# Kernel optimization log

Measured on AMD Instinct MI355X. Metric: run time of the kernel, lower is better.

## Reference

```python
import jax, jax.numpy as jnp
import numpy as np

H, DH = 8, 64
DIM = 512
INNER = H * DH
GAMMA = 0.01
LAMBDA_REG = 0.001


def _ln(x, g, b, eps=1e-5):
    mu = x.mean(-1, keepdims=True)
    var = x.var(-1, keepdims=True)  # ddof=0, matches torch LayerNorm
    return (x - mu) / jnp.sqrt(var + eps) * g + b


def _proj(x, ln_g, ln_b, W):
    # LayerNorm -> Linear(no bias) -> split heads: [Q,N,DIM] -> [H,Q,N,DH]
    Q, N, _ = x.shape
    y = _ln(x, ln_g, ln_b) @ W
    return jnp.transpose(y.reshape(Q, N, H, DH), (2, 0, 1, 3))


def setup_inputs() -> dict:
    key = jax.random.key(0)
    ks = jax.random.split(key, 10)
    s = 0.02
    return {
        "q": jax.random.normal(ks[0], (16, 512, DIM), jnp.float32),
        "k": jax.random.normal(ks[1], (16, 512, DIM), jnp.float32),
        "v": jax.random.normal(ks[2], (16, 512, DIM), jnp.float32),
        "ln_g": jnp.ones((DIM,), jnp.float32),
        "ln_b": jnp.zeros((DIM,), jnp.float32),
        "W_in": jax.random.normal(ks[3], (DIM, INNER), jnp.float32) * s,
        "wp1_w": jax.random.normal(ks[4], (2 * DH, DH), jnp.float32) * s,
        "wp1_b": jnp.zeros((DH,), jnp.float32),
        "wpln_g": jnp.ones((DH,), jnp.float32),
        "wpln_b": jnp.zeros((DH,), jnp.float32),
        "wp2_w": jax.random.normal(ks[5], (DH, DH // 2), jnp.float32) * s,
        "wp2_b": jnp.zeros((DH // 2,), jnp.float32),
        "wp3_w": jax.random.normal(ks[6], (DH // 2, 3), jnp.float32) * s,
        "wp3_b": jnp.zeros((3,), jnp.float32),
        "temp": jnp.ones((1,), jnp.float32) * 5.0,
        "W_out": jax.random.normal(ks[7], (INNER, DIM), jnp.float32) * s,
        "b_out": jnp.zeros((DIM,), jnp.float32),
    }


def reference(q, k, v, ln_g, ln_b, W_in, wp1_w, wp1_b, wpln_g, wpln_b,
              wp2_w, wp2_b, wp3_w, wp3_b, temp, W_out, b_out):
    sg = jax.lax.stop_gradient
    std1 = lambda x: jnp.std(x, ddof=1)  # torch.std is unbiased

    f_q = _proj(q, ln_g, ln_b, W_in)  # [H,Q,N,DH]
    f_k = _proj(k, ln_g, ln_b, W_in)  # [H,Q,M,DH]
    f_v = _proj(v, ln_g, ln_b, W_in)
    m = f_k.shape[2]

    # --- cosine similarity component (cosine_distance + extra clamp) ---
    dots_raw = jnp.einsum('hqnd,hqmd->hqnm', f_q, f_k)
    n1 = jnp.linalg.norm(f_q, axis=-1, keepdims=True) + 1e-8          # [H,Q,N,1]
    n2 = jnp.linalg.norm(f_k, axis=-1, keepdims=True) + 1e-8          # [H,Q,M,1]
    cosine_sim = jnp.clip(dots_raw / (n1 * jnp.swapaxes(n2, -1, -2)), -0.99, 0.99)

    # --- regularized covariance component ---
    f_kc = f_k - f_k.mean(axis=2, keepdims=True)
    f_qc = f_q - f_q.mean(axis=-1, keepdims=True)
    cov = jnp.einsum('hqnd,hqmd->hqnm', f_qc, f_kc) / (DH ** 0.5 + 1e-8)
    cov = jnp.clip((LAMBDA_REG / max(m, 1)) * cov, -10.0, 10.0)

    # --- margin-based variance component (eval mode: adaptive_gamma == GAMMA) ---
    fqn = f_q / jnp.maximum(jnp.linalg.norm(f_q, axis=-1, keepdims=True), 1e-8)
    fkn = f_k / jnp.maximum(jnp.linalg.norm(f_k, axis=-1, keepdims=True), 1e-8)
    cs = jnp.clip(jnp.einsum('hqnd,hqmd->hqnm', fqn, fkn), -0.99, 0.99)
    margin = jnp.clip(GAMMA - cs, 0.0, 2.0)
    var_comp = jnp.broadcast_to(margin.mean(-1, keepdims=True), cs.shape)

    # --- dynamic weight predictor (dropouts identity in eval) ---
    qg = f_q.mean(axis=(1, 2))                 # [H,DH]
    kg = f_k.mean(axis=(1, 2))
    feats = jnp.concatenate([qg, kg], axis=-1)  # [H,2*DH]
    h1 = jax.nn.relu(_ln(feats @ wp1_w + wp1_b, wpln_g, wpln_b))
    h2 = jax.nn.relu(h1 @ wp2_w + wp2_b)
    logits = jax.nn.softmax(h2 @ wp3_w + wp3_b, axis=-1)  # softmax inside Sequential
    weights = jax.nn.softmax(logits / jnp.clip(temp, 0.1, 20.0), axis=-1)  # [H,3]
    cos_w = weights[:, 0].reshape(H, 1, 1, 1)
    cov_w = weights[:, 1].reshape(H, 1, 1, 1)
    var_w = weights[:, 2].reshape(H, 1, 1, 1)

    # --- global-std rescale + mix + adaptive temperature ---
    cos_s = cosine_sim / (sg(std1(cosine_sim)) + 1e-8)
    cov_s = cov / (sg(std1(cov)) + 1e-8) * 0.1
    var_s = var_comp / (sg(std1(var_comp)) + 1e-8) * 0.1
    dots = cos_w * cos_s + cov_w * cov_s + var_w * var_s
    attn_t = 1.0 + 0.5 * sg(std1(dots))
    dots = dots / jnp.clip(attn_t, 0.5, 5.0)

    out = jnp.einsum('hqnm,hqmd->hqnd', jax.nn.softmax(dots, axis=-1), f_v)
    out = jnp.transpose(out, (1, 2, 0, 3)).reshape(q.shape[0], q.shape[1], INNER)
    return out @ W_out + b_out
```

## Files before the change

### kernel.cpp

```cpp
#include <hip/hip_runtime.h>
#include <math.h>

#define NH 8
#define DHD 64
#define DMODEL 512
#define QB 16
#define SEQ 512
#define NROWS (QB*SEQ)
#define NHQ (NH*QB)
#define KCOV ((float)((0.001/512.0)/(8.0+1e-8)))

typedef __attribute__((ext_vector_type(8))) short short8;
typedef __attribute__((ext_vector_type(8))) unsigned short ushort8v;
typedef __attribute__((ext_vector_type(4))) unsigned short ushort4v;
typedef __attribute__((ext_vector_type(4))) float f32x4;

__device__ __forceinline__ float bf2f(unsigned short u){
  union { unsigned int i; float f; } c; c.i = ((unsigned int)u)<<16; return c.f;
}
__device__ __forceinline__ unsigned short f2bf(float f){
  union { float f; unsigned int i; } c; c.f = f;
  unsigned int u = c.i;
  u += 0x7fffu + ((u>>16)&1u);
  return (unsigned short)(u>>16);
}
__device__ __forceinline__ unsigned cvtpk(float a, float b){
  unsigned r; asm("v_cvt_pk_bf16_f32 %0, %1, %2" : "=v"(r) : "v"(a), "v"(b)); return r;
}
__device__ __forceinline__ float clampf(float x, float lo, float hi){ return fminf(fmaxf(x,lo),hi); }

__device__ __forceinline__ f32x4 MFMA(short8 a, short8 b, f32x4 c){
  return __builtin_amdgcn_mfma_f32_16x16x32_bf16(a, b, c, 0, 0, 0);
}
__device__ __forceinline__ short8 frag_ld(const unsigned short* T, int row, int rowbytes, int kbyte){
  int addr = row*rowbytes + (kbyte ^ ((row&7)<<4));
  return *reinterpret_cast<const short8*>(reinterpret_cast<const char*>(T) + addr);
}
__device__ __forceinline__ void tile_st16(unsigned short* T, int row, int rowbytes, int kbyte, ushort8v v){
  int addr = row*rowbytes + (kbyte ^ ((row&7)<<4));
  *reinterpret_cast<ushort8v*>(reinterpret_cast<char*>(T) + addr) = v;
}
__device__ __forceinline__ void tile_st8(unsigned short* T, int row, int rowbytes, int kbyte, ushort4v v){
  int addr = row*rowbytes + (kbyte ^ ((row&7)<<4));
  *reinterpret_cast<ushort4v*>(reinterpret_cast<char*>(T) + addr) = v;
}

__global__ void __launch_bounds__(256) prep_kernel(
    const float* __restrict__ xq, const float* __restrict__ xk, const float* __restrict__ xv,
    const float* __restrict__ Wi, const float* __restrict__ Wo,
    float* __restrict__ mu, float* __restrict__ rstd,
    unsigned short* __restrict__ WiT, unsigned short* __restrict__ WoT)
{
  __shared__ float T[64][68];
  int b = blockIdx.x, t = threadIdx.x;
  if (b < 6144){
    int which = b >> 11, rowblk = b & 2047;
    const float* src = which==0 ? xq : (which==1 ? xk : xv);
    int w = t >> 6, lane = t & 63;
    int row = rowblk*4 + w;
    const float* x = src + (size_t)row*DMODEL;
    float4 v1 = *reinterpret_cast<const float4*>(&x[lane*8]);
    float4 v2 = *reinterpret_cast<const float4*>(&x[lane*8+4]);
    float s  = v1.x+v1.y+v1.z+v1.w + v2.x+v2.y+v2.z+v2.w;
    float ss = v1.x*v1.x+v1.y*v1.y+v1.z*v1.z+v1.w*v1.w
             + v2.x*v2.x+v2.y*v2.y+v2.z*v2.z+v2.w*v2.w;
    #pragma unroll
    for (int m=32; m>0; m>>=1){ s += __shfl_xor(s,m,64); ss += __shfl_xor(ss,m,64); }
    if (lane==0){
      float m_ = s*(1.0f/DMODEL);
      float var = ss*(1.0f/DMODEL) - m_*m_;
      mu[(size_t)which*NROWS + row]   = m_;
      rstd[(size_t)which*NROWS + row] = rsqrtf(var + 1e-5f);
    }
  } else {
    int wb = b - 6144;
    const float* src = (wb>=64) ? Wo : Wi;
    unsigned short* dst = (wb>=64) ? WoT : WiT;
    int rc = wb & 63;
    int r0 = (rc>>3)*64, c0 = (rc&7)*64;
    for (int it=0; it<4; ++it){
      int idx = it*256+t, row = idx>>4, q = idx&15;
      float4 v = *reinterpret_cast<const float4*>(&src[(size_t)(r0+row)*DMODEL + c0 + q*4]);
      T[row][q*4+0]=v.x; T[row][q*4+1]=v.y; T[row][q*4+2]=v.z; T[row][q*4+3]=v.w;
    }
    __syncthreads();
    for (int it=0; it<4; ++it){
      int idx = it*256+t, oc = idx>>4, q = idx&15;
      ushort4v o;
      o[0]=f2bf(T[q*4+0][oc]); o[1]=f2bf(T[q*4+1][oc]);
      o[2]=f2bf(T[q*4+2][oc]); o[3]=f2bf(T[q*4+3][oc]);
      *reinterpret_cast<ushort4v*>(&dst[(size_t)(c0+oc)*DMODEL + r0 + q*4]) = o;
    }
  }
}

__global__ void __launch_bounds__(256) proj_mfma_kernel(
    const float* __restrict__ xq, const float* __restrict__ xk, const float* __restrict__ xv,
    const float* __restrict__ g, const float* __restrict__ bb,
    const unsigned short* __restrict__ WiT,
    const float* __restrict__ mu, const float* __restrict__ rstd,
    unsigned short* __restrict__ fq, unsigned short* __restrict__ fk, unsigned short* __restrict__ fvT,
    float* __restrict__ aqA, float* __restrict__ i1qA,
    float* __restrict__ rskA, float* __restrict__ i1kA)
{
  int which = blockIdx.z;
  const float* src = which==0?xq:(which==1?xk:xv);
  int r0 = blockIdx.x*128;
  int c0 = blockIdx.y*128;
  __shared__ unsigned short XT[128*64];
  __shared__ unsigned short WT[128*64];
  __shared__ float gs[DMODEL], bs[DMODEL], mus[128], rss[128];
  int t = threadIdx.x;
  for (int i=t;i<DMODEL;i+=256){ gs[i]=g[i]; bs[i]=bb[i]; }
  if (t<128){ mus[t]=mu[(size_t)which*NROWS+r0+t]; rss[t]=rstd[(size_t)which*NROWS+r0+t]; }
  int w=t>>6, lane=t&63, l16=lane&15, lh=lane>>4;
  f32x4 acc[4][4];
  #pragma unroll
  for(int i=0;i<4;i++){ for(int j=0;j<4;j++) acc[i][j]=(f32x4){0.f,0.f,0.f,0.f}; }
  for (int k0=0;k0<DMODEL;k0+=64){
    __syncthreads();
    for (int it=0; it<8; ++it){
      int idx=it*256+t, row=idx>>4, q=idx&15;
      float4 x4 = *reinterpret_cast<const float4*>(&src[(size_t)(r0+row)*DMODEL + k0 + q*4]);
      float m_=mus[row], rs_=rss[row];
      const float* g4=&gs[k0+q*4]; const float* b4=&bs[k0+q*4];
      ushort4v o;
      o[0]=f2bf((x4.x-m_)*rs_*g4[0]+b4[0]);
      o[1]=f2bf((x4.y-m_)*rs_*g4[1]+b4[1]);
      o[2]=f2bf((x4.z-m_)*rs_*g4[2]+b4[2]);
      o[3]=f2bf((x4.w-m_)*rs_*g4[3]+b4[3]);
      tile_st8(XT, row, 128, q*8, o);
    }
    for (int it=0; it<4; ++it){
      int idx=it*256+t, row=idx>>3, q=idx&7;
      ushort8v v = *reinterpret_cast<const ushort8v*>(&WiT[(size_t)(c0+row)*DMODEL + k0 + q*8]);
      tile_st16(WT, row, 128, q*16, v);
    }
    __syncthreads();
    if (which<2){
      int dr=(w&1)*64, nc=(w>>1)*64;
      #pragma unroll
      for (int ks=0; ks<2; ++ks){
        int kb = lh*16 + ks*64;
        short8 a[4], b[4];
        #pragma unroll
        for (int i=0;i<4;i++) a[i] = frag_ld(WT, dr+i*16+l16, 128, kb);
        #pragma unroll
        for (int j=0;j<4;j++) b[j] = frag_ld(XT, nc+j*16+l16, 128, kb);
        #pragma unroll
        for (int i=0;i<4;i++){
          #pragma unroll
          for (int j=0;j<4;j++) acc[i][j]=MFMA(a[i],b[j],acc[i][j]);
        }
      }
    } else {
      int nr=(w>>1)*64, dc=(w&1)*64;
      #pragma unroll
      for (int ks=0; ks<2; ++ks){
        int kb = lh*16 + ks*64;
        short8 a[4], b[4];
        #pragma unroll
        for (int i=0;i<4;i++) a[i] = frag_ld(XT, nr+i*16+l16, 128, kb);
        #pragma unroll
        for (int j=0;j<4;j++) b[j] = frag_ld(WT, dc+j*16+l16, 128, kb);
        #pragma unroll
        for (int i=0;i<4;i++){
          #pragma unroll
          for (int j=0;j<4;j++) acc[i][j]=MFMA(a[i],b[j],acc[i][j]);
        }
      }
    }
  }
  if (which<2){
    unsigned short* dst = which ? fk : fq;
    int dr=(w&1)*64, nc=(w>>1)*64;
    #pragma unroll
    for (int i=0;i<4;i++){
      #pragma unroll
      for (int j=0;j<4;j++){
        int cl = c0 + dr + i*16 + lh*4;
        int ng = r0 + nc + j*16 + l16;
        int head = cl>>6, dd = cl&63;
        int hq = head*QB + (ng>>9);
        int n = ng&511;
        ushort4v o;
        o[0]=f2bf(acc[i][j][0]); o[1]=f2bf(acc[i][j][1]);
        o[2]=f2bf(acc[i][j][2]); o[3]=f2bf(acc[i][j][3]);
        *reinterpret_cast<ushort4v*>(&dst[((size_t)hq*SEQ+n)*DHD + dd]) = o;
      }
    }
    int head = (c0>>6) + (w&1);
    #pragma unroll
    for (int j=0;j<4;j++){
      float s=0.f, ss=0.f;
      #pragma unroll
      for (int i=0;i<4;i++){
        #pragma unroll
        for (int r=0;r<4;r++){ float x = acc[i][j][r]; s += x; ss = fmaf(x,x,ss); }
      }
      s += __shfl_xor(s,16,64); ss += __shfl_xor(ss,16,64);
      s += __shfl_xor(s,32,64); ss += __shfl_xor(ss,32,64);
      if (lh==0){
        int ng = r0 + nc + j*16 + l16;
        int hq = head*QB + (ng>>9);
        int n = ng&511;
        float nrm = sqrtf(ss);
        if (which==0){
          aqA[hq*SEQ+n]  = s*(1.0f/64.0f);
          i1qA[hq*SEQ+n] = 1.0f/(nrm+1e-8f);
        } else {
          rskA[hq*SEQ+n] = s;
          i1kA[hq*SEQ+n] = 1.0f/(nrm+1e-8f);
        }
      }
    }
  } else {
    int nr=(w>>1)*64, dc=(w&1)*64;
    #pragma unroll
    for (int i=0;i<4;i++){
      #pragma unroll
      for (int j=0;j<4;j++){
        int ngb = r0 + nr + i*16 + lh*4;
        int dg  = c0 + dc + j*16 + l16;
        int head = dg>>6, dd = dg&63;
        int hq = head*QB + (ngb>>9);
        int n = ngb&511;
        ushort4v o;
        o[0]=f2bf(acc[i][j][0]); o[1]=f2bf(acc[i][j][1]);
        o[2]=f2bf(acc[i][j][2]); o[3]=f2bf(acc[i][j][3]);
        *reinterpret_cast<ushort4v*>(&fvT[((size_t)hq*DHD+dd)*SEQ + n]) = o;
      }
    }
  }
}

__global__ void __launch_bounds__(256) colsum_kernel(
    const unsigned short* __restrict__ fq, const unsigned short* __restrict__ fk,
    float* __restrict__ colpart)
{
  int hq = blockIdx.x, quarter = blockIdx.y, isk = blockIdx.z;
  const unsigned short* F = (isk ? fk : fq) + (size_t)hq*SEQ*DHD;
  int t = threadIdx.x, g = t&15, rg = t>>4;
  float acc0=0.f, acc1=0.f, acc2=0.f, acc3=0.f;
  #pragma unroll
  for (int i=0;i<8;i++){
    int r = quarter*128 + rg + 16*i;
    ushort4v v = *reinterpret_cast<const ushort4v*>(&F[(size_t)r*DHD + g*4]);
    acc0+=bf2f(v[0]); acc1+=bf2f(v[1]); acc2+=bf2f(v[2]); acc3+=bf2f(v[3]);
  }
  __shared__ float sh[16][68];
  sh[rg][g*4+0]=acc0; sh[rg][g*4+1]=acc1; sh[rg][g*4+2]=acc2; sh[rg][g*4+3]=acc3;
  __syncthreads();
  if (t<64){
    float s=0.f;
    #pragma unroll
    for (int r=0;r<16;r++) s += sh[r][t];
    colpart[(((size_t)isk*NHQ + hq)*4 + quarter)*64 + t] = s;
  }
}

__global__ void __launch_bounds__(64) colreduce_kernel(
    const float* __restrict__ colpart,
    float* __restrict__ qgp, float* __restrict__ kgp, float* __restrict__ c2A)
{
  int hq = blockIdx.x, d = threadIdx.x;
  float sq=0.f, sk=0.f;
  #pragma unroll
  for (int qu=0;qu<4;qu++){
    sq += colpart[(((size_t)0*NHQ + hq)*4 + qu)*64 + d];
    sk += colpart[(((size_t)1*NHQ + hq)*4 + qu)*64 + d];
  }
  qgp[hq*64+d]=sq; kgp[hq*64+d]=sk;
  float c = sk*(1.0f/512.0f);
  #pragma unroll
  for (int m=32;m>0;m>>=1) c += __shfl_xor(c,m,64);
  if (d==0) c2A[hq]=c;
}

__global__ void __launch_bounds__(256) score_m1_kernel(
    const unsigned short* __restrict__ fq, const unsigned short* __restrict__ fk,
    const float* __restrict__ aqA, const float* __restrict__ i1qA,
    const float* __restrict__ rskA, const float* __restrict__ i1kA,
    const float* __restrict__ c2A, const float* __restrict__ kgp,
    float* __restrict__ c1A, float* __restrict__ rmaxcA, float* __restrict__ rmaxoA,
    float* __restrict__ momf, double* __restrict__ varp)
{
  int strip=blockIdx.x, q_=blockIdx.y, h=blockIdx.z;
  int hq=h*QB+q_, n0=strip*64;
  const unsigned short* Fq=fq+(size_t)hq*SEQ*DHD;
  const unsigned short* Fk=fk+(size_t)hq*SEQ*DHD;
  __shared__ unsigned short KT[128*64];
  __shared__ float red[256];
  __shared__ double dred[256];
  int t=threadIdx.x, w=t>>6, lane=t&63, l16=lane&15, lh=lane>>4;
  int n = n0 + w*16 + l16;
  float c2v = c2A[hq];
  float aqv = aqA[hq*SEQ+n];
  float iq1 = i1qA[hq*SEQ+n];
  short8 qa[2];
  #pragma unroll
  for (int ks=0;ks<2;ks++)
    qa[ks] = *reinterpret_cast<const short8*>(&Fq[(size_t)n*DHD + ks*32 + lh*8]);
  float c1v = 0.f;
  #pragma unroll
  for (int ks=0;ks<2;ks++){
    const float* bkp = &kgp[hq*64 + ks*32 + lh*8];
    float4 b0 = *reinterpret_cast<const float4*>(bkp);
    float4 b1 = *reinterpret_cast<const float4*>(bkp+4);
    float bb[8] = {b0.x,b0.y,b0.z,b0.w,b1.x,b1.y,b1.z,b1.w};
    #pragma unroll
    for (int i=0;i<8;i++) c1v = fmaf(bf2f((unsigned short)qa[ks][i]), bb[i], c1v);
  }
  c1v *= (1.0f/512.0f);
  c1v += __shfl_xor(c1v,16,64);
  c1v += __shfl_xor(c1v,32,64);
  if (lane<16) c1A[hq*SEQ+n] = c1v;
  float c1x = KCOV*(c1v - aqv*c2v);
  float aqx = KCOV*aqv;
  float sc=0.f,sc2=0.f,so=0.f,so2=0.f,sco=0.f;
  float rc=0.f, ro=0.f, rm=0.f, rmc=-1e30f, rmo=-1e30f;
  for (int mc=0;mc<4;mc++){
    int m0=mc*128;
    __syncthreads();
    for (int it=0;it<4;++it){
      int idx=it*256+t, row=idx>>3, qc=idx&7;
      ushort8v vv = *reinterpret_cast<const ushort8v*>(&Fk[(size_t)(m0+row)*DHD + qc*8]);
      tile_st16(KT,row,128,qc*16,vv);
    }
    __syncthreads();
    #pragma unroll
    for (int mh=0;mh<2;mh++){
      int mb = mh*64;
      f32x4 acc[4];
      #pragma unroll
      for (int mf=0;mf<4;mf++) acc[mf]=(f32x4){0.f,0.f,0.f,0.f};
      #pragma unroll
      for (int mf=0;mf<4;mf++){
        #pragma unroll
        for (int ks=0;ks<2;ks++){
          short8 kf = frag_ld(KT, mb+mf*16+l16, 128, lh*16+ks*64);
          acc[mf] = MFMA(kf, qa[ks], acc[mf]);
        }
      }
      #pragma unroll
      for (int mf=0;mf<4;mf++){
        int mg = hq*SEQ + m0 + mb + mf*16 + lh*4;
        float4 rsk4 = *reinterpret_cast<const float4*>(&rskA[mg]);
        float4 i1k4 = *reinterpret_cast<const float4*>(&i1kA[mg]);
        float rk[4]={rsk4.x,rsk4.y,rsk4.z,rsk4.w};
        float ik[4]={i1k4.x,i1k4.y,i1k4.z,i1k4.w};
        #pragma unroll
        for (int r=0;r<4;r++){
          float S = acc[mf][r];
          float cosv = clampf(S*iq1*ik[r], -0.99f, 0.99f);
          float u = fmaf(KCOV, S, -c1x);
          float covv = fmaf(-aqx, rk[r], u);
          covv = clampf(covv, -10.0f, 10.0f);
          float marg = clampf(0.01f - cosv, 0.0f, 2.0f);
          sc += cosv; sc2 = fmaf(cosv,cosv,sc2);
          so += covv; so2 = fmaf(covv,covv,so2);
          sco = fmaf(cosv,covv,sco);
          rc += cosv; ro += covv; rm += marg;
          rmc = fmaxf(rmc, cosv); rmo = fmaxf(rmo, covv);
        }
      }
    }
  }
  rc += __shfl_xor(rc,16,64); rc += __shfl_xor(rc,32,64);
  ro += __shfl_xor(ro,16,64); ro += __shfl_xor(ro,32,64);
  rm += __shfl_xor(rm,16,64); rm += __shfl_xor(rm,32,64);
  rmc = fmaxf(rmc, __shfl_xor(rmc,16,64)); rmc = fmaxf(rmc, __shfl_xor(rmc,32,64));
  rmo = fmaxf(rmo, __shfl_xor(rmo,16,64)); rmo = fmaxf(rmo, __shfl_xor(rmo,32,64));
  if (lane<16){
    rmaxcA[hq*SEQ+n] = rmc;
    rmaxoA[hq*SEQ+n] = rmo;
  }
  double vm=0.0, vm2=0.0, vmc=0.0, vmo=0.0;
  if (lane<16){
    float mm = rm*(1.0f/512.0f);
    vm  = (double)mm;
    vm2 = (double)mm*(double)mm;
    vmc = (double)mm*(double)rc;
    vmo = (double)mm*(double)ro;
  }
  float fs[5]={sc,sc2,so,so2,sco};
  for (int c=0;c<5;c++){
    __syncthreads();
    red[t]=fs[c]; __syncthreads();
    for (int o=128;o>0;o>>=1){ if (t<o) red[t]+=red[t+o]; __syncthreads(); }
    if (t==0) momf[(size_t)(hq*8+strip)*5 + c] = red[0];
  }
  double ds[4]={vm,vm2,vmc,vmo};
  for (int c=0;c<4;c++){
    __syncthreads();
    dred[t]=ds[c]; __syncthreads();
    for (int o=128;o>0;o>>=1){ if (t<o) dred[t]+=dred[t+o]; __syncthreads(); }
    if (t==0) varp[(size_t)(hq*8+strip)*4 + c] = dred[0];
  }
}

__global__ void __launch_bounds__(256) finalize_kernel(
    const float* __restrict__ qgp, const float* __restrict__ kgp,
    const float* __restrict__ wp1w, const float* __restrict__ wp1b,
    const float* __restrict__ wplg, const float* __restrict__ wplb,
    const float* __restrict__ wp2w, const float* __restrict__ wp2b,
    const float* __restrict__ wp3w, const float* __restrict__ wp3b,
    const float* __restrict__ temp,
    const float* __restrict__ momf, const double* __restrict__ varp,
    float* __restrict__ params)
{
  int t = threadIdx.x;
  __shared__ float feats[8][128];
  __shared__ float h1s[8][64];
  __shared__ float h2s[8][32];
  __shared__ float wts[8][3];
  __shared__ double Sh[8][9];
  for (int idx=t; idx<512; idx+=256){
    int h = idx>>6, d = idx&63;
    float s1=0, s2=0;
    for (int qq=0; qq<QB; qq++){ s1 += qgp[(h*QB+qq)*64+d]; s2 += kgp[(h*QB+qq)*64+d]; }
    feats[h][d]    = s1*(1.0f/8192.0f);
    feats[h][64+d] = s2*(1.0f/8192.0f);
  }
  __syncthreads();
  int w = t>>6, j = t&63;
  for (int pp=0; pp<2; pp++){
    int h = w + pp*4;
    float acc = wp1b[j];
    for (int k=0;k<128;k++) acc += feats[h][k]*wp1w[k*64+j];
    float s=acc, s2=acc*acc;
    #pragma unroll
    for (int m=32;m>0;m>>=1){ s+=__shfl_xor(s,m,64); s2+=__shfl_xor(s2,m,64); }
    float mean = s*(1.0f/64.0f);
    float var  = s2*(1.0f/64.0f) - mean*mean;
    float xh = (acc-mean)*rsqrtf(var+1e-5f)*wplg[j] + wplb[j];
    h1s[h][j] = fmaxf(xh, 0.0f);
  }
  __syncthreads();
  {
    int h = t>>5, j2 = t&31;
    float acc = wp2b[j2];
    for (int k=0;k<64;k++) acc += h1s[h][k]*wp2w[k*32+j2];
    h2s[h][j2] = fmaxf(acc, 0.0f);
  }
  __syncthreads();
  if (t<8){
    int h = t;
    float z[3] = {wp3b[0], wp3b[1], wp3b[2]};
    for (int k=0;k<32;k++){
      float hv = h2s[h][k];
      z[0]+=hv*wp3w[k*3]; z[1]+=hv*wp3w[k*3+1]; z[2]+=hv*wp3w[k*3+2];
    }
    float mx = fmaxf(z[0], fmaxf(z[1], z[2]));
    float e0=expf(z[0]-mx), e1=expf(z[1]-mx), e2=expf(z[2]-mx);
    float inv = 1.0f/(e0+e1+e2);
    float l0=e0*inv, l1=e1*inv, l2=e2*inv;
    float tv = temp[0]; tv = fminf(fmaxf(tv, 0.1f), 20.0f);
    float y0=l0/tv, y1=l1/tv, y2=l2/tv;
    float mx2 = fmaxf(y0, fmaxf(y1, y2));
    float f0=expf(y0-mx2), f1=expf(y1-mx2), f2=expf(y2-mx2);
    float inv2 = 1.0f/(f0+f1+f2);
    wts[h][0]=f0*inv2; wts[h][1]=f1*inv2; wts[h][2]=f2*inv2;
  }
  __syncthreads();
  if (t<40){
    int h = t/5, c = t%5;
    double s = 0;
    for (int e=0; e<128; e++) s += (double)momf[(size_t)(h*128+e)*5 + c];
    Sh[h][c] = s;
  }
  __syncthreads();
  if (t<32){
    int h = t>>2, c = t&3;
    double s = 0;
    for (int e=0; e<128; e++) s += varp[(size_t)(h*128+e)*4 + c];
    Sh[h][5+c] = s;
  }
  __syncthreads();
  if (t==0){
    const double Ntot = 33554432.0;
    double T1c=0,T2c=0,T1o=0,T2o=0,T1v=0,T2v=0;
    for (int h=0;h<8;h++){
      T1c+=Sh[h][0]; T2c+=Sh[h][1]; T1o+=Sh[h][2]; T2o+=Sh[h][3];
      T1v+=512.0*Sh[h][5]; T2v+=512.0*Sh[h][6];
    }
    double stdc = sqrt(fmax((T2c - T1c*T1c/Ntot)/(Ntot-1.0), 0.0));
    double stdo = sqrt(fmax((T2o - T1o*T1o/Ntot)/(Ntot-1.0), 0.0));
    double stdv = sqrt(fmax((T2v - T1v*T1v/Ntot)/(Ntot-1.0), 0.0));
    double ah[8], bh[8];
    double Sd1=0, Sd2=0;
    for (int h=0;h<8;h++){
      double a = (double)wts[h][0]/(stdc+1e-8);
      double b = (double)wts[h][1]*0.1/(stdo+1e-8);
      double c = (double)wts[h][2]*0.1/(stdv+1e-8);
      ah[h]=a; bh[h]=b;
      Sd1 += a*Sh[h][0] + b*Sh[h][2] + c*512.0*Sh[h][5];
      Sd2 += a*a*Sh[h][1] + b*b*Sh[h][3] + c*c*512.0*Sh[h][6]
           + 2.0*a*b*Sh[h][4] + 2.0*a*c*Sh[h][7] + 2.0*b*c*Sh[h][8];
    }
    double stdd = sqrt(fmax((Sd2 - Sd1*Sd1/Ntot)/(Ntot-1.0), 0.0));
    double att = 1.0 + 0.5*stdd;
    att = fmin(fmax(att, 0.5), 5.0);
    double scale = 1.0/att;
    for (int h=0;h<8;h++){
      params[h*2+0] = (float)(scale*ah[h]);
      params[h*2+1] = (float)(scale*bh[h]);
    }
  }
}

__global__ void __launch_bounds__(256) attn_m2_kernel(
    const unsigned short* __restrict__ fq, const unsigned short* __restrict__ fk,
    const unsigned short* __restrict__ fvT,
    const float* __restrict__ aqA, const float* __restrict__ c1A, const float* __restrict__ i1qA,
    const float* __restrict__ rskA, const float* __restrict__ i1kA,
    const float* __restrict__ c2A, const float* __restrict__ params,
    const float* __restrict__ rmaxcA, const float* __restrict__ rmaxoA,
    unsigned short* __restrict__ attn_bf)
{
  int strip=blockIdx.x, q_=blockIdx.y, h=blockIdx.z;
  int hq=h*QB+q_, n0=strip*64;
  const unsigned short* Fq=fq+(size_t)hq*SEQ*DHD;
  const unsigned short* Fk=fk+(size_t)hq*SEQ*DHD;
  const unsigned short* FvT=fvT+(size_t)hq*DHD*SEQ;
  __shared__ unsigned short KT[128*64];
  __shared__ unsigned short VT[64*128];
  __shared__ unsigned short P[64*64];
  int t=threadIdx.x, w=t>>6, lane=t&63, l16=lane&15, lh=lane>>4;
  int n = n0 + w*16 + l16;
  float c2v=c2A[hq];
  float pa=params[h*2], pb=params[h*2+1];
  float aqv = aqA[hq*SEQ+n];
  float c1v = c1A[hq*SEQ+n];
  float iq1 = i1qA[hq*SEQ+n];
  float rmc = rmaxcA[hq*SEQ+n];
  float rmo = rmaxoA[hq*SEQ+n];
  float pbk = pb*KCOV;
  float ra  = pa*iq1;
  float bndc = 0.99f*pa;
  float rowc = -pbk*(c1v - aqv*c2v);
  float r3   = pbk*aqv;
  float Mrow = fmaf(pa, rmc, pb*rmo);
  short8 qa[2];
  #pragma unroll
  for (int ks=0;ks<2;ks++)
    qa[ks] = *reinterpret_cast<const short8*>(&Fq[(size_t)n*DHD + ks*32 + lh*8]);
  short8 ones;
  #pragma unroll
  for (int i=0;i<8;i++) ones[i] = (short)0x3F80;
  f32x4 accO[4];
  #pragma unroll
  for (int j=0;j<4;j++) accO[j]=(f32x4){0.f,0.f,0.f,0.f};
  f32x4 den = (f32x4){0.f,0.f,0.f,0.f};
  for (int mc=0;mc<4;mc++){
    int m0=mc*128;
    __syncthreads();
    for (int it=0;it<4;++it){
      int idx=it*256+t, row=idx>>3, qc=idx&7;
      ushort8v vv = *reinterpret_cast<const ushort8v*>(&Fk[(size_t)(m0+row)*DHD + qc*8]);
      tile_st16(KT,row,128,qc*16,vv);
    }
    for (int it=0;it<4;++it){
      int idx=it*256+t, dd=idx>>4, c=idx&15;
      ushort8v vv=*reinterpret_cast<const ushort8v*>(&FvT[(size_t)dd*SEQ + m0 + c*8]);
      tile_st16(VT, dd, 256, c*16, vv);
    }
    __syncthreads();
    #pragma unroll
    for (int mh=0;mh<2;mh++){
      int mb = mh*64;
      f32x4 acc[4];
      #pragma unroll
      for (int mf=0;mf<4;mf++) acc[mf]=(f32x4){0.f,0.f,0.f,0.f};
      #pragma unroll
      for (int mf=0;mf<4;mf++){
        #pragma unroll
        for (int ks=0;ks<2;ks++){
          short8 kf = frag_ld(KT, mb+mf*16+l16, 128, lh*16+ks*64);
          acc[mf] = MFMA(kf, qa[ks], acc[mf]);
        }
      }
      int prow = w*16 + l16;
      #pragma unroll
      for (int mf=0;mf<4;mf++){
        int mg = hq*SEQ + m0 + mb + mf*16 + lh*4;
        float4 rsk4 = *reinterpret_cast<const float4*>(&rskA[mg]);
        float4 i1k4 = *reinterpret_cast<const float4*>(&i1kA[mg]);
        float rk[4]={rsk4.x,rsk4.y,rsk4.z,rsk4.w};
        float ik[4]={i1k4.x,i1k4.y,i1k4.z,i1k4.w};
        #pragma unroll
        for (int r=0;r<4;r++){
          float S = acc[mf][r];
          float tt = S*ra; tt *= ik[r];
          float cc = clampf(tt, -bndc, bndc);
          float u = fmaf(pbk, S, rowc);
          float lin = fmaf(-r3, rk[r], u);
          acc[mf][r] = __expf(cc + lin - Mrow);
        }
        unsigned lo = cvtpk(acc[mf][0], acc[mf][1]);
        unsigned hi = cvtpk(acc[mf][2], acc[mf][3]);
        int pbyte = (mf*32 + lh*8) ^ ((prow&7)<<4);
        *reinterpret_cast<uint2*>(reinterpret_cast<char*>(P) + prow*128 + pbyte)
          = make_uint2(lo, hi);
      }
      #pragma unroll
      for (int ks=0;ks<2;ks++){
        short8 pfrag = frag_ld(P, prow, 128, lh*16 + ks*64);
        #pragma unroll
        for (int dcf=0;dcf<4;dcf++){
          short8 vb = frag_ld(VT, dcf*16+l16, 256, mb*2 + ks*64 + lh*16);
          accO[dcf] = MFMA(pfrag, vb, accO[dcf]);
        }
        den = MFMA(pfrag, ones, den);
      }
    }
  }
  f32x4 invD;
  #pragma unroll
  for (int r=0;r<4;r++) invD[r] = 1.0f/den[r];
  #pragma unroll
  for (int dcf=0;dcf<4;dcf++){
    #pragma unroll
    for (int r=0;r<4;r++){
      int row = w*16 + lh*4 + r;
      int col = dcf*16 + l16;
      int addr = row*128 + ((col*2) ^ ((row&7)<<4));
      *reinterpret_cast<unsigned short*>(reinterpret_cast<char*>(P) + addr)
        = f2bf(accO[dcf][r]*invD[r]);
    }
  }
  __syncthreads();
  for (int it=0; it<2; ++it){
    int idx = it*256 + t;
    int row = idx>>3, c = idx&7;
    int addr = row*128 + ((c*16) ^ ((row&7)<<4));
    ushort8v vv = *reinterpret_cast<ushort8v*>(reinterpret_cast<char*>(P) + addr);
    *reinterpret_cast<ushort8v*>(
      &attn_bf[(size_t)(q_*SEQ + n0 + row)*DMODEL + h*DHD + c*8]) = vv;
  }
}

__global__ void __launch_bounds__(256) out_mfma_kernel(
    const unsigned short* __restrict__ attn_bf, const unsigned short* __restrict__ WoT,
    const float* __restrict__ bias, float* __restrict__ out)
{
  int r0=blockIdx.x*128;
  int c0=blockIdx.y*128;
  __shared__ unsigned short AT[128*64];
  __shared__ unsigned short WT[128*64];
  int t=threadIdx.x, w=t>>6, lane=t&63, l16=lane&15, lh=lane>>4;
  f32x4 acc[4][4];
  #pragma unroll
  for(int i=0;i<4;i++){ for(int j=0;j<4;j++) acc[i][j]=(f32x4){0.f,0.f,0.f,0.f}; }
  for (int k0=0;k0<DMODEL;k0+=64){
    __syncthreads();
    for (int it=0; it<4; ++it){
      int idx=it*256+t, row=idx>>3, q=idx&7;
      ushort8v v = *reinterpret_cast<const ushort8v*>(&attn_bf[(size_t)(r0+row)*DMODEL + k0 + q*8]);
      tile_st16(AT, row, 128, q*16, v);
    }
    for (int it=0; it<4; ++it){
      int idx=it*256+t, row=idx>>3, q=idx&7;
      ushort8v v = *reinterpret_cast<const ushort8v*>(&WoT[(size_t)(c0+row)*DMODEL + k0 + q*8]);
      tile_st16(WT, row, 128, q*16, v);
    }
    __syncthreads();
    int nr=(w&1)*64, mr=(w>>1)*64;
    #pragma unroll
    for (int ks=0; ks<2; ++ks){
      int kb = lh*16 + ks*64;
      short8 a[4], b[4];
      #pragma unroll
      for (int i=0;i<4;i++) a[i] = frag_ld(WT, nr+i*16+l16, 128, kb);
      #pragma unroll
      for (int j=0;j<4;j++) b[j] = frag_ld(AT, mr+j*16+l16, 128, kb);
      #pragma unroll
      for (int i=0;i<4;i++){
        #pragma unroll
        for (int j=0;j<4;j++) acc[i][j]=MFMA(a[i],b[j],acc[i][j]);
      }
    }
  }
  #pragma unroll
  for (int i=0;i<4;i++){
    int nb = c0+(w&1)*64+i*16+lh*4;
    float4 b4 = *reinterpret_cast<const float4*>(&bias[nb]);
    #pragma unroll
    for (int j=0;j<4;j++){
      int mg = r0+(w>>1)*64+j*16+l16;
      f32x4 o = acc[i][j];
      o[0]+=b4.x; o[1]+=b4.y; o[2]+=b4.z; o[3]+=b4.w;
      *reinterpret_cast<f32x4*>(&out[(size_t)mg*DMODEL + nb]) = o;
    }
  }
}

extern "C" void kernel_launch(void* const* d_in, const int* in_sizes, int n_in,
                              void* d_out, int out_size, void* d_ws, size_t ws_size,
                              hipStream_t stream)
{
  (void)in_sizes; (void)n_in; (void)out_size; (void)ws_size;
  const float* q     = (const float*)d_in[0];
  const float* k     = (const float*)d_in[1];
  const float* v     = (const float*)d_in[2];
  const float* ln_g  = (const float*)d_in[3];
  const float* ln_b  = (const float*)d_in[4];
  const float* W_in  = (const float*)d_in[5];
  const float* wp1w  = (const float*)d_in[6];
  const float* wp1b  = (const float*)d_in[7];
  const float* wplg  = (const float*)d_in[8];
  const float* wplb  = (const float*)d_in[9];
  const float* wp2w  = (const float*)d_in[10];
  const float* wp2b  = (const float*)d_in[11];
  const float* wp3w  = (const float*)d_in[12];
  const float* wp3b  = (const float*)d_in[13];
  const float* temp  = (const float*)d_in[14];
  const float* W_out = (const float*)d_in[15];
  const float* b_out = (const float*)d_in[16];
  float* out = (float*)d_out;

  char* wsb = (char*)d_ws;
  size_t off = 0;
  auto alloc = [&](size_t bytes)->char*{
    char* p = wsb + off; off += (bytes + 255) & ~(size_t)255; return p;
  };
  unsigned short* fq_b   = (unsigned short*)alloc((size_t)NHQ*SEQ*DHD*2);
  unsigned short* fk_b   = (unsigned short*)alloc((size_t)NHQ*SEQ*DHD*2);
  unsigned short* fvT_b  = (unsigned short*)alloc((size_t)NHQ*SEQ*DHD*2);
  unsigned short* attn_b = (unsigned short*)alloc((size_t)NROWS*DMODEL*2);
  unsigned short* WiT    = (unsigned short*)alloc((size_t)DMODEL*DMODEL*2);
  unsigned short* WoT    = (unsigned short*)alloc((size_t)DMODEL*DMODEL*2);
  float* mu     = (float*)alloc(3*NROWS*4);
  float* rstd   = (float*)alloc(3*NROWS*4);
  float* aqA    = (float*)alloc(NHQ*SEQ*4);
  float* c1A    = (float*)alloc(NHQ*SEQ*4);
  float* i1qA   = (float*)alloc(NHQ*SEQ*4);
  float* rskA   = (float*)alloc(NHQ*SEQ*4);
  float* i1kA   = (float*)alloc(NHQ*SEQ*4);
  float* rmaxcA = (float*)alloc(NHQ*SEQ*4);
  float* rmaxoA = (float*)alloc(NHQ*SEQ*4);
  float* c2A    = (float*)alloc(NHQ*4);
  float* qgp    = (float*)alloc(NHQ*64*4);
  float* kgp    = (float*)alloc(NHQ*64*4);
  float* colpart= (float*)alloc((size_t)2*NHQ*4*64*4);
  float* momf   = (float*)alloc((size_t)NHQ*8*5*4);
  double* varp  = (double*)alloc((size_t)NHQ*8*4*8);
  float* params = (float*)alloc(64);

  prep_kernel<<<6272, 256, 0, stream>>>(q, k, v, W_in, W_out, mu, rstd, WiT, WoT);
  proj_mfma_kernel<<<dim3(64,4,3), 256, 0, stream>>>(q, k, v, ln_g, ln_b, WiT, mu, rstd,
                                                     fq_b, fk_b, fvT_b, aqA, i1qA, rskA, i1kA);
  colsum_kernel<<<dim3(NHQ, 4, 2), 256, 0, stream>>>(fq_b, fk_b, colpart);
  colreduce_kernel<<<dim3(NHQ), 64, 0, stream>>>(colpart, qgp, kgp, c2A);
  score_m1_kernel<<<dim3(8, QB, NH), 256, 0, stream>>>(fq_b, fk_b, aqA, i1qA, rskA, i1kA,
                                                       c2A, kgp, c1A, rmaxcA, rmaxoA, momf, varp);
  finalize_kernel<<<1, 256, 0, stream>>>(qgp, kgp, wp1w, wp1b, wplg, wplb, wp2w, wp2b,
                                         wp3w, wp3b, temp, momf, varp, params);
  attn_m2_kernel<<<dim3(8, QB, NH), 256, 0, stream>>>(fq_b, fk_b, fvT_b, aqA, c1A, i1qA,
                                                      rskA, i1kA, c2A, params, rmaxcA, rmaxoA, attn_b);
  out_mfma_kernel<<<dim3(64,4), 256, 0, stream>>>(attn_b, WoT, b_out, out);
}
```

Before: 173.9 us.

## Precompute bf16 LayerNorm activations in prep, merge colsum kernels, stage key stats in LDS

The prep kernel now applies LayerNorm and writes bf16 normalized rows, so the projection GEMM loads half-size bf16 tiles instead of re-reading fp32 inputs once per column block and normalizing them there. The column-sum and column-reduce kernels are merged into one kernel that reduces a whole head in a single block, removing one launch and a partial buffer. The score and attention kernels copy the per-key rsk/i1k vectors into shared memory once instead of reading them from global memory inside the inner loop. The cost is an extra bf16 activation buffer written and read through global memory, and fewer blocks in the column-stat kernel.

```diff
diff --git a/kernel.cpp b/kernel.cpp
--- a/kernel.cpp
+++ b/kernel.cpp
@@ -40,15 +40,12 @@
   int addr = row*rowbytes + (kbyte ^ ((row&7)<<4));
   *reinterpret_cast<ushort8v*>(reinterpret_cast<char*>(T) + addr) = v;
 }
-__device__ __forceinline__ void tile_st8(unsigned short* T, int row, int rowbytes, int kbyte, ushort4v v){
-  int addr = row*rowbytes + (kbyte ^ ((row&7)<<4));
-  *reinterpret_cast<ushort4v*>(reinterpret_cast<char*>(T) + addr) = v;
-}
 
 __global__ void __launch_bounds__(256) prep_kernel(
     const float* __restrict__ xq, const float* __restrict__ xk, const float* __restrict__ xv,
+    const float* __restrict__ ln_g, const float* __restrict__ ln_b,
     const float* __restrict__ Wi, const float* __restrict__ Wo,
-    float* __restrict__ mu, float* __restrict__ rstd,
+    unsigned short* __restrict__ xln,
     unsigned short* __restrict__ WiT, unsigned short* __restrict__ WoT)
 {
   __shared__ float T[64][68];
@@ -66,12 +63,23 @@
              + v2.x*v2.x+v2.y*v2.y+v2.z*v2.z+v2.w*v2.w;
     #pragma unroll
     for (int m=32; m>0; m>>=1){ s += __shfl_xor(s,m,64); ss += __shfl_xor(ss,m,64); }
-    if (lane==0){
-      float m_ = s*(1.0f/DMODEL);
-      float var = ss*(1.0f/DMODEL) - m_*m_;
-      mu[(size_t)which*NROWS + row]   = m_;
-      rstd[(size_t)which*NROWS + row] = rsqrtf(var + 1e-5f);
-    }
+    float m_ = s*(1.0f/DMODEL);
+    float var = ss*(1.0f/DMODEL) - m_*m_;
+    float r_ = rsqrtf(var + 1e-5f);
+    float4 g1 = *reinterpret_cast<const float4*>(&ln_g[lane*8]);
+    float4 g2 = *reinterpret_cast<const float4*>(&ln_g[lane*8+4]);
+    float4 b1 = *reinterpret_cast<const float4*>(&ln_b[lane*8]);
+    float4 b2 = *reinterpret_cast<const float4*>(&ln_b[lane*8+4]);
+    ushort8v o;
+    o[0]=f2bf((v1.x-m_)*r_*g1.x + b1.x);
+    o[1]=f2bf((v1.y-m_)*r_*g1.y + b1.y);
+    o[2]=f2bf((v1.z-m_)*r_*g1.z + b1.z);
+    o[3]=f2bf((v1.w-m_)*r_*g1.w + b1.w);
+    o[4]=f2bf((v2.x-m_)*r_*g2.x + b2.x);
+    o[5]=f2bf((v2.y-m_)*r_*g2.y + b2.y);
+    o[6]=f2bf((v2.z-m_)*r_*g2.z + b2.z);
+    o[7]=f2bf((v2.w-m_)*r_*g2.w + b2.w);
+    *reinterpret_cast<ushort8v*>(&xln[((size_t)which*NROWS + row)*DMODEL + lane*8]) = o;
   } else {
     int wb = b - 6144;
     const float* src = (wb>=64) ? Wo : Wi;
@@ -95,41 +103,29 @@
 }
 
 __global__ void __launch_bounds__(256) proj_mfma_kernel(
-    const float* __restrict__ xq, const float* __restrict__ xk, const float* __restrict__ xv,
-    const float* __restrict__ g, const float* __restrict__ bb,
+    const unsigned short* __restrict__ xln,
     const unsigned short* __restrict__ WiT,
-    const float* __restrict__ mu, const float* __restrict__ rstd,
     unsigned short* __restrict__ fq, unsigned short* __restrict__ fk, unsigned short* __restrict__ fvT,
     float* __restrict__ aqA, float* __restrict__ i1qA,
     float* __restrict__ rskA, float* __restrict__ i1kA)
 {
   int which = blockIdx.z;
-  const float* src = which==0?xq:(which==1?xk:xv);
+  const unsigned short* src = xln + (size_t)which*NROWS*DMODEL;
   int r0 = blockIdx.x*128;
   int c0 = blockIdx.y*128;
   __shared__ unsigned short XT[128*64];
   __shared__ unsigned short WT[128*64];
-  __shared__ float gs[DMODEL], bs[DMODEL], mus[128], rss[128];
   int t = threadIdx.x;
-  for (int i=t;i<DMODEL;i+=256){ gs[i]=g[i]; bs[i]=bb[i]; }
-  if (t<128){ mus[t]=mu[(size_t)which*NROWS+r0+t]; rss[t]=rstd[(size_t)which*NROWS+r0+t]; }
   int w=t>>6, lane=t&63, l16=lane&15, lh=lane>>4;
   f32x4 acc[4][4];
   #pragma unroll
   for(int i=0;i<4;i++){ for(int j=0;j<4;j++) acc[i][j]=(f32x4){0.f,0.f,0.f,0.f}; }
   for (int k0=0;k0<DMODEL;k0+=64){
     __syncthreads();
-    for (int it=0; it<8; ++it){
-      int idx=it*256+t, row=idx>>4, q=idx&15;
-      float4 x4 = *reinterpret_cast<const float4*>(&src[(size_t)(r0+row)*DMODEL + k0 + q*4]);
-      float m_=mus[row], rs_=rss[row];
-      const float* g4=&gs[k0+q*4]; const float* b4=&bs[k0+q*4];
-      ushort4v o;
-      o[0]=f2bf((x4.x-m_)*rs_*g4[0]+b4[0]);
-      o[1]=f2bf((x4.y-m_)*rs_*g4[1]+b4[1]);
-      o[2]=f2bf((x4.z-m_)*rs_*g4[2]+b4[2]);
-      o[3]=f2bf((x4.w-m_)*rs_*g4[3]+b4[3]);
-      tile_st8(XT, row, 128, q*8, o);
+    for (int it=0; it<4; ++it){
+      int idx=it*256+t, row=idx>>3, q=idx&7;
+      ushort8v v = *reinterpret_cast<const ushort8v*>(&src[(size_t)(r0+row)*DMODEL + k0 + q*8]);
+      tile_st16(XT, row, 128, q*16, v);
     }
     for (int it=0; it<4; ++it){
       int idx=it*256+t, row=idx>>3, q=idx&7;
@@ -234,17 +230,17 @@
   }
 }
 
-__global__ void __launch_bounds__(256) colsum_kernel(
+__global__ void __launch_bounds__(256) colstat_kernel(
     const unsigned short* __restrict__ fq, const unsigned short* __restrict__ fk,
-    float* __restrict__ colpart)
+    float* __restrict__ qgp, float* __restrict__ kgp, float* __restrict__ c2A)
 {
-  int hq = blockIdx.x, quarter = blockIdx.y, isk = blockIdx.z;
+  int hq = blockIdx.x, isk = blockIdx.y;
   const unsigned short* F = (isk ? fk : fq) + (size_t)hq*SEQ*DHD;
   int t = threadIdx.x, g = t&15, rg = t>>4;
   float acc0=0.f, acc1=0.f, acc2=0.f, acc3=0.f;
-  #pragma unroll
-  for (int i=0;i<8;i++){
-    int r = quarter*128 + rg + 16*i;
+  #pragma unroll 4
+  for (int i=0;i<32;i++){
+    int r = rg + 16*i;
     ushort4v v = *reinterpret_cast<const ushort4v*>(&F[(size_t)r*DHD + g*4]);
     acc0+=bf2f(v[0]); acc1+=bf2f(v[1]); acc2+=bf2f(v[2]); acc3+=bf2f(v[3]);
   }
@@ -255,26 +251,16 @@
     float s=0.f;
     #pragma unroll
     for (int r=0;r<16;r++) s += sh[r][t];
-    colpart[(((size_t)isk*NHQ + hq)*4 + quarter)*64 + t] = s;
-  }
-}
-
-__global__ void __launch_bounds__(64) colreduce_kernel(
-    const float* __restrict__ colpart,
-    float* __restrict__ qgp, float* __restrict__ kgp, float* __restrict__ c2A)
-{
-  int hq = blockIdx.x, d = threadIdx.x;
-  float sq=0.f, sk=0.f;
-  #pragma unroll
-  for (int qu=0;qu<4;qu++){
-    sq += colpart[(((size_t)0*NHQ + hq)*4 + qu)*64 + d];
-    sk += colpart[(((size_t)1*NHQ + hq)*4 + qu)*64 + d];
-  }
-  qgp[hq*64+d]=sq; kgp[hq*64+d]=sk;
-  float c = sk*(1.0f/512.0f);
-  #pragma unroll
-  for (int m=32;m>0;m>>=1) c += __shfl_xor(c,m,64);
-  if (d==0) c2A[hq]=c;
+    if (isk){
+      kgp[hq*64+t]=s;
+      float c = s*(1.0f/512.0f);
+      #pragma unroll
+      for (int m=32;m>0;m>>=1) c += __shfl_xor(c,m,64);
+      if (t==0) c2A[hq]=c;
+    } else {
+      qgp[hq*64+t]=s;
+    }
+  }
 }
 
 __global__ void __launch_bounds__(256) score_m1_kernel(
@@ -290,10 +276,12 @@
   const unsigned short* Fq=fq+(size_t)hq*SEQ*DHD;
   const unsigned short* Fk=fk+(size_t)hq*SEQ*DHD;
   __shared__ unsigned short KT[128*64];
+  __shared__ float rskL[512], i1kL[512];
   __shared__ float red[256];
   __shared__ double dred[256];
   int t=threadIdx.x, w=t>>6, lane=t&63, l16=lane&15, lh=lane>>4;
   int n = n0 + w*16 + l16;
+  for (int i=t;i<512;i+=256){ rskL[i]=rskA[hq*SEQ+i]; i1kL[i]=i1kA[hq*SEQ+i]; }
   float c2v = c2A[hq];
   float aqv = aqA[hq*SEQ+n];
   float iq1 = i1qA[hq*SEQ+n];
@@ -344,9 +332,9 @@
       }
       #pragma unroll
       for (int mf=0;mf<4;mf++){
-        int mg = hq*SEQ + m0 + mb + mf*16 + lh*4;
-        float4 rsk4 = *reinterpret_cast<const float4*>(&rskA[mg]);
-        float4 i1k4 = *reinterpret_cast<const float4*>(&i1kA[mg]);
+        int ml = m0 + mb + mf*16 + lh*4;
+        float4 rsk4 = *reinterpret_cast<const float4*>(&rskL[ml]);
+        float4 i1k4 = *reinterpret_cast<const float4*>(&i1kL[ml]);
         float rk[4]={rsk4.x,rsk4.y,rsk4.z,rsk4.w};
         float ik[4]={i1k4.x,i1k4.y,i1k4.z,i1k4.w};
         #pragma unroll
@@ -526,8 +514,10 @@
   __shared__ unsigned short KT[128*64];
   __shared__ unsigned short VT[64*128];
   __shared__ unsigned short P[64*64];
+  __shared__ float rskL[512], i1kL[512];
   int t=threadIdx.x, w=t>>6, lane=t&63, l16=lane&15, lh=lane>>4;
   int n = n0 + w*16 + l16;
+  for (int i=t;i<512;i+=256){ rskL[i]=rskA[hq*SEQ+i]; i1kL[i]=i1kA[hq*SEQ+i]; }
   float c2v=c2A[hq];
   float pa=params[h*2], pb=params[h*2+1];
   float aqv = aqA[hq*SEQ+n];
@@ -583,9 +573,9 @@
       int prow = w*16 + l16;
       #pragma unroll
       for (int mf=0;mf<4;mf++){
-        int mg = hq*SEQ + m0 + mb + mf*16 + lh*4;
-        float4 rsk4 = *reinterpret_cast<const float4*>(&rskA[mg]);
-        float4 i1k4 = *reinterpret_cast<const float4*>(&i1kA[mg]);
+        int ml = m0 + mb + mf*16 + lh*4;
+        float4 rsk4 = *reinterpret_cast<const float4*>(&rskL[ml]);
+        float4 i1k4 = *reinterpret_cast<const float4*>(&i1kL[ml]);
         float rk[4]={rsk4.x,rsk4.y,rsk4.z,rsk4.w};
         float ik[4]={i1k4.x,i1k4.y,i1k4.z,i1k4.w};
         #pragma unroll
@@ -724,14 +714,13 @@
   auto alloc = [&](size_t bytes)->char*{
     char* p = wsb + off; off += (bytes + 255) & ~(size_t)255; return p;
   };
+  unsigned short* xln    = (unsigned short*)alloc((size_t)3*NROWS*DMODEL*2);
   unsigned short* fq_b   = (unsigned short*)alloc((size_t)NHQ*SEQ*DHD*2);
   unsigned short* fk_b   = (unsigned short*)alloc((size_t)NHQ*SEQ*DHD*2);
   unsigned short* fvT_b  = (unsigned short*)alloc((size_t)NHQ*SEQ*DHD*2);
   unsigned short* attn_b = (unsigned short*)alloc((size_t)NROWS*DMODEL*2);
   unsigned short* WiT    = (unsigned short*)alloc((size_t)DMODEL*DMODEL*2);
   unsigned short* WoT    = (unsigned short*)alloc((size_t)DMODEL*DMODEL*2);
-  float* mu     = (float*)alloc(3*NROWS*4);
-  float* rstd   = (float*)alloc(3*NROWS*4);
   float* aqA    = (float*)alloc(NHQ*SEQ*4);
   float* c1A    = (float*)alloc(NHQ*SEQ*4);
   float* i1qA   = (float*)alloc(NHQ*SEQ*4);
@@ -742,16 +731,14 @@
   float* c2A    = (float*)alloc(NHQ*4);
   float* qgp    = (float*)alloc(NHQ*64*4);
   float* kgp    = (float*)alloc(NHQ*64*4);
-  float* colpart= (float*)alloc((size_t)2*NHQ*4*64*4);
   float* momf   = (float*)alloc((size_t)NHQ*8*5*4);
   double* varp  = (double*)alloc((size_t)NHQ*8*4*8);
   float* params = (float*)alloc(64);
 
-  prep_kernel<<<6272, 256, 0, stream>>>(q, k, v, W_in, W_out, mu, rstd, WiT, WoT);
-  proj_mfma_kernel<<<dim3(64,4,3), 256, 0, stream>>>(q, k, v, ln_g, ln_b, WiT, mu, rstd,
-                                                     fq_b, fk_b, fvT_b, aqA, i1qA, rskA, i1kA);
-  colsum_kernel<<<dim3(NHQ, 4, 2), 256, 0, stream>>>(fq_b, fk_b, colpart);
-  colreduce_kernel<<<dim3(NHQ), 64, 0, stream>>>(colpart, qgp, kgp, c2A);
+  prep_kernel<<<6272, 256, 0, stream>>>(q, k, v, ln_g, ln_b, W_in, W_out, xln, WiT, WoT);
+  proj_mfma_kernel<<<dim3(64,4,3), 256, 0, stream>>>(xln, WiT, fq_b, fk_b, fvT_b,
+                                                     aqA, i1qA, rskA, i1kA);
+  colstat_kernel<<<dim3(NHQ, 2), 256, 0, stream>>>(fq_b, fk_b, qgp, kgp, c2A);
   score_m1_kernel<<<dim3(8, QB, NH), 256, 0, stream>>>(fq_b, fk_b, aqA, i1qA, rskA, i1kA,
                                                        c2A, kgp, c1A, rmaxcA, rmaxoA, momf, varp);
   finalize_kernel<<<1, 256, 0, stream>>>(qgp, kgp, wp1w, wp1b, wplg, wplb, wp2w, wp2b,
```

Result: faster. 169.6 us (-2.5%).
